# Kernel optimization log

Hardware: AMD Instinct MI355X
Metric: run time of the kernel (lower is better)

Reference implementation:

```python
import jax, jax.numpy as jnp
import numpy as np

EPS = 1e-6
ENERGY_THRESHOLD = 0.95
LS_INIT = 1e-5


def setup_inputs() -> dict:
    key = jax.random.key(0)
    k_x, k_u, k_s, k_v = jax.random.split(key, 4)
    dim, max_rank = 4096, 16
    x = jax.random.normal(k_x, (4, 2048, dim), dtype=jnp.float32)
    U = jax.random.normal(k_u, (dim, max_rank), dtype=jnp.float32) * 0.02
    S = jax.random.uniform(k_s, (max_rank,), dtype=jnp.float32)
    V = jax.random.normal(k_v, (max_rank, dim), dtype=jnp.float32) * 0.02
    norm_weight = jnp.ones((dim,), dtype=jnp.float32)
    gamma = jnp.full((dim,), LS_INIT, dtype=jnp.float32)
    return {"x": x, "U": U, "S": S, "V": V,
            "norm_weight": norm_weight, "gamma": gamma}


def _rank_mask(S):
    # Effective rank from singular-value energy (non-differentiable decision,
    # matching torch's .item() host sync which detaches it from autograd).
    s_abs = jnp.abs(S)
    cum = jnp.cumsum(s_abs) / jnp.maximum(s_abs.sum(), 1e-8)
    hit = cum >= ENERGY_THRESHOLD
    r = jnp.where(hit.any(), jnp.argmax(hit) + 1, S.shape[0])
    keep = (jnp.arange(S.shape[0]) < r).astype(S.dtype)
    return jax.lax.stop_gradient(keep)


def reference(x, U, S, V, norm_weight, gamma):
    # RMSNorm (computed in fp32, matching x.float() in torch)
    xf = x.astype(jnp.float32)
    x_norm = (xf * jax.lax.rsqrt(jnp.mean(xf * xf, axis=-1, keepdims=True) + EPS)).astype(x.dtype)
    x_norm = x_norm * norm_weight
    # Adaptive-rank low-rank projection: masking columns >= r equals slicing [:r]
    keep = _rank_mask(S)
    h = jnp.einsum('bsd,dr->bsr', x_norm, U)        # [B,S,max_rank]
    h = h * (S * keep)                               # zero out ranks >= r
    h = jnp.einsum('bsr,rd->bsd', h, V)             # [B,S,dim]
    # LayerScale + residual
    return x + h * gamma
```

## Files before the change

kernel.cpp:

```cpp
#include <hip/hip_runtime.h>

#define DIM   4096
#define RANK  16
#define BM    16
#define NT    1024
#define NWAVE 16
#define KSLICE (DIM/NWAVE)
#define NKB   (KSLICE/32)
#define NCB   (DIM/16/NWAVE)

typedef __fp16 f16;
typedef __fp16 half4 __attribute__((ext_vector_type(4)));
typedef __fp16 half8 __attribute__((ext_vector_type(8)));
typedef float  floatx4 __attribute__((ext_vector_type(4)));

__global__ __launch_bounds__(256) void prep_weights(const float* __restrict__ U,
    const float* __restrict__ nw, const float* __restrict__ V,
    f16* __restrict__ Ub, f16* __restrict__ Vb)
{
    const int i   = blockIdx.x * 256 + threadIdx.x;
    const int l   = i & 63;
    const int n   = l & 15;
    const int blk = l >> 4;
    if (i < 8192) {
        const int kb = i >> 6;
        half8 u;
        #pragma unroll
        for (int e = 0; e < 8; ++e) {
            const int k = kb * 32 + blk * 8 + e;
            u[e] = (f16)(nw[k] * U[(size_t)k * RANK + n]);
        }
        *(half8*)(Ub + (size_t)i * 8) = u;
    }
    {
        const int cb = i >> 6;
        half4 v;
        #pragma unroll
        for (int e = 0; e < 4; ++e) {
            const int k = blk * 4 + e;
            v[e] = (f16)V[(size_t)k * DIM + cb * 16 + n];
        }
        *(half4*)(Vb + (size_t)i * 4) = v;
    }
}

__global__ __launch_bounds__(NT, 8) void arl_fused(
    const float* __restrict__ x,  const f16* __restrict__ Ub,
    const f16* __restrict__ Vb,   const float* __restrict__ S,
    const float* __restrict__ gamma, float* __restrict__ out)
{
    const int t   = threadIdx.x;
    const int w   = t >> 6;
    const int l   = t & 63;
    const int n   = l & 15;
    const int blk = l >> 4;
    const size_t row0 = (size_t)blockIdx.x * BM;

    __shared__ float s_hacc[NWAVE][16][17];
    __shared__ float s_ssq[NWAVE][16];
    __shared__ __align__(8) f16 s_hh[16][16];

    const float* xlane = x + (row0 + n) * DIM + w * KSLICE + blk * 8;
    const half8* UbW   = (const half8*)Ub + (size_t)w * NKB * 64 + l;

    floatx4 acc = {0.f, 0.f, 0.f, 0.f};
    float ssq = 0.f;

    #pragma unroll
    for (int kb = 0; kb < NKB; ++kb) {
        const float4 xa0 = *(const float4*)(xlane + kb * 32);
        const float4 xa1 = *(const float4*)(xlane + kb * 32 + 4);
        const half8  ub  = UbW[(size_t)kb * 64];
        ssq = fmaf(xa0.x, xa0.x, ssq); ssq = fmaf(xa0.y, xa0.y, ssq);
        ssq = fmaf(xa0.z, xa0.z, ssq); ssq = fmaf(xa0.w, xa0.w, ssq);
        ssq = fmaf(xa1.x, xa1.x, ssq); ssq = fmaf(xa1.y, xa1.y, ssq);
        ssq = fmaf(xa1.z, xa1.z, ssq); ssq = fmaf(xa1.w, xa1.w, ssq);
        half8 a;
        a[0] = (f16)xa0.x; a[1] = (f16)xa0.y; a[2] = (f16)xa0.z; a[3] = (f16)xa0.w;
        a[4] = (f16)xa1.x; a[5] = (f16)xa1.y; a[6] = (f16)xa1.z; a[7] = (f16)xa1.w;
        acc = __builtin_amdgcn_mfma_f32_16x16x32_f16(a, ub, acc, 0, 0, 0);
    }

    ssq += __shfl_xor(ssq, 16, 64);
    ssq += __shfl_xor(ssq, 32, 64);
    if (l < 16) s_ssq[w][l] = ssq;

    #pragma unroll
    for (int j = 0; j < 4; ++j) s_hacc[w][blk * 4 + j][n] = acc[j];
    __syncthreads();

    if (t < 256) {
        const int m = t >> 4, q = t & 15;
        float hsum = 0.f, tssq = 0.f;
        #pragma unroll
        for (int ww = 0; ww < NWAVE; ++ww) {
            hsum += s_hacc[ww][m][q];
            tssq += s_ssq[ww][m];
        }
        const float rstd = rsqrtf(tssq * (1.0f / DIM) + 1e-6f);
        float tot = 0.f;
        #pragma unroll
        for (int i = 0; i < RANK; ++i) tot += fabsf(S[i]);
        const float denom = fmaxf(tot, 1e-8f);
        float cum = 0.f, se = 0.f;
        #pragma unroll
        for (int i = 0; i < RANK; ++i) {
            if (i == q) se = ((cum / denom) < 0.95f) ? S[i] : 0.f;
            cum += fabsf(S[i]);
        }
        s_hh[m][q] = (f16)(hsum * se * rstd);
    }
    __syncthreads();

    const half4 ah = *(const half4*)&s_hh[n][blk * 4];
    const half4* Vb4 = (const half4*)Vb;
    const floatx4 zero = {0.f, 0.f, 0.f, 0.f};

    #pragma unroll 2
    for (int i = 0; i < NCB; ++i) {
        const int cb = w * NCB + i;
        const int c0 = cb * 16;
        const half4 bv = Vb4[(size_t)cb * 64 + l];
        floatx4 d = __builtin_amdgcn_mfma_f32_16x16x16f16(ah, bv, zero, 0, 0, 0);
        const float g = gamma[c0 + n];
        const float* xr  = x   + (row0 + blk * 4) * DIM + c0 + n;
        float*       orr = out + (row0 + blk * 4) * DIM + c0 + n;
        #pragma unroll
        for (int j = 0; j < 4; ++j) {
            const float xv = xr[(size_t)j * DIM];
            __builtin_nontemporal_store(fmaf(g, d[j], xv), orr + (size_t)j * DIM);
        }
    }
}

extern "C" void kernel_launch(void* const* d_in, const int* in_sizes, int n_in,
                              void* d_out, int out_size, void* d_ws, size_t ws_size,
                              hipStream_t stream) {
    (void)in_sizes; (void)n_in; (void)ws_size;
    const float* x  = (const float*)d_in[0];
    const float* U  = (const float*)d_in[1];
    const float* S  = (const float*)d_in[2];
    const float* V  = (const float*)d_in[3];
    const float* nw = (const float*)d_in[4];
    const float* g  = (const float*)d_in[5];
    float* out = (float*)d_out;
    f16* Ub = (f16*)d_ws;
    f16* Vb = (f16*)((char*)d_ws + 128 * 1024);

    hipLaunchKernelGGL(prep_weights, dim3(64), dim3(256), 0, stream,
                       U, nw, V, Ub, Vb);

    const int rows = out_size / DIM;
    const int grid = rows / BM;
    hipLaunchKernelGGL(arl_fused, dim3(grid), dim3(NT), 0, stream,
                       x, Ub, Vb, S, g, out);
}
```

Baseline: 77.37 us.

## Process two row tiles per block, overlapping second projection with first output phase

Each block now handles two 16-row tiles. The reduction loads and MFMA for the second tile are interleaved with the V-projection and residual write of the first tile, so memory traffic and compute from both phases overlap. The output phase also switches to swapped MFMA operands, which lets each lane use float4 loads and stores of x, gamma and out. The grid is halved and the occupancy hint drops from 8 to 4. This risks lower occupancy and more register pressure, and it adds a third barrier.

```diff
diff --git a/kernel.cpp b/kernel.cpp
--- a/kernel.cpp
+++ b/kernel.cpp
@@ -3,16 +3,16 @@
 #define DIM   4096
 #define RANK  16
 #define BM    16
+#define TPB   2
 #define NT    1024
 #define NWAVE 16
-#define KSLICE (DIM/NWAVE)
-#define NKB   (KSLICE/32)
-#define NCB   (DIM/16/NWAVE)
 
 typedef __fp16 f16;
 typedef __fp16 half4 __attribute__((ext_vector_type(4)));
 typedef __fp16 half8 __attribute__((ext_vector_type(8)));
 typedef float  floatx4 __attribute__((ext_vector_type(4)));
+
+#define SCHED_FENCE() __builtin_amdgcn_sched_barrier(0)
 
 __global__ __launch_bounds__(256) void prep_weights(const float* __restrict__ U,
     const float* __restrict__ nw, const float* __restrict__ V,
@@ -44,7 +44,7 @@
     }
 }
 
-__global__ __launch_bounds__(NT, 8) void arl_fused(
+__global__ __launch_bounds__(NT, 4) void arl_fused(
     const float* __restrict__ x,  const f16* __restrict__ Ub,
     const f16* __restrict__ Vb,   const float* __restrict__ S,
     const float* __restrict__ gamma, float* __restrict__ out)
@@ -54,23 +54,27 @@
     const int l   = t & 63;
     const int n   = l & 15;
     const int blk = l >> 4;
-    const size_t row0 = (size_t)blockIdx.x * BM;
+    const size_t rowB = (size_t)blockIdx.x * (BM * TPB);
 
     __shared__ float s_hacc[NWAVE][16][17];
     __shared__ float s_ssq[NWAVE][16];
-    __shared__ __align__(8) f16 s_hh[16][16];
-
-    const float* xlane = x + (row0 + n) * DIM + w * KSLICE + blk * 8;
-    const half8* UbW   = (const half8*)Ub + (size_t)w * NKB * 64 + l;
+    __shared__ __align__(8) f16 s_hh[TPB][16][16];
+
+    const half4* Vb4 = (const half4*)Vb;
+    const floatx4 zero = {0.f, 0.f, 0.f, 0.f};
+
+    const float* xlaneT0 = x + (rowB + n) * DIM + w * 256 + blk * 8;
+    const float* xlaneT1 = xlaneT0 + (size_t)BM * DIM;
+    const f16*   UbW     = Ub + ((size_t)(w * 8) * 64 + l) * 8;
 
     floatx4 acc = {0.f, 0.f, 0.f, 0.f};
     float ssq = 0.f;
 
     #pragma unroll
-    for (int kb = 0; kb < NKB; ++kb) {
-        const float4 xa0 = *(const float4*)(xlane + kb * 32);
-        const float4 xa1 = *(const float4*)(xlane + kb * 32 + 4);
-        const half8  ub  = UbW[(size_t)kb * 64];
+    for (int i = 0; i < 8; ++i) {
+        const float4 xa0 = *(const float4*)(xlaneT0 + i * 32);
+        const float4 xa1 = *(const float4*)(xlaneT0 + i * 32 + 4);
+        const half8  ub  = *(const half8*)(UbW + (size_t)i * 512);
         ssq = fmaf(xa0.x, xa0.x, ssq); ssq = fmaf(xa0.y, xa0.y, ssq);
         ssq = fmaf(xa0.z, xa0.z, ssq); ssq = fmaf(xa0.w, xa0.w, ssq);
         ssq = fmaf(xa1.x, xa1.x, ssq); ssq = fmaf(xa1.y, xa1.y, ssq);
@@ -80,13 +84,14 @@
         a[4] = (f16)xa1.x; a[5] = (f16)xa1.y; a[6] = (f16)xa1.z; a[7] = (f16)xa1.w;
         acc = __builtin_amdgcn_mfma_f32_16x16x32_f16(a, ub, acc, 0, 0, 0);
     }
-
-    ssq += __shfl_xor(ssq, 16, 64);
-    ssq += __shfl_xor(ssq, 32, 64);
-    if (l < 16) s_ssq[w][l] = ssq;
-
-    #pragma unroll
-    for (int j = 0; j < 4; ++j) s_hacc[w][blk * 4 + j][n] = acc[j];
+    {
+        float sq = ssq;
+        sq += __shfl_xor(sq, 16, 64);
+        sq += __shfl_xor(sq, 32, 64);
+        if (l < 16) s_ssq[w][l] = sq;
+        #pragma unroll
+        for (int j = 0; j < 4; ++j) s_hacc[w][blk * 4 + j][n] = acc[j];
+    }
     __syncthreads();
 
     if (t < 256) {
@@ -108,27 +113,102 @@
             if (i == q) se = ((cum / denom) < 0.95f) ? S[i] : 0.f;
             cum += fabsf(S[i]);
         }
-        s_hh[m][q] = (f16)(hsum * se * rstd);
-    }
-    __syncthreads();
-
-    const half4 ah = *(const half4*)&s_hh[n][blk * 4];
-    const half4* Vb4 = (const half4*)Vb;
-    const floatx4 zero = {0.f, 0.f, 0.f, 0.f};
-
-    #pragma unroll 2
-    for (int i = 0; i < NCB; ++i) {
-        const int cb = w * NCB + i;
-        const int c0 = cb * 16;
-        const half4 bv = Vb4[(size_t)cb * 64 + l];
-        floatx4 d = __builtin_amdgcn_mfma_f32_16x16x16f16(ah, bv, zero, 0, 0, 0);
-        const float g = gamma[c0 + n];
-        const float* xr  = x   + (row0 + blk * 4) * DIM + c0 + n;
-        float*       orr = out + (row0 + blk * 4) * DIM + c0 + n;
-        #pragma unroll
-        for (int j = 0; j < 4; ++j) {
-            const float xv = xr[(size_t)j * DIM];
-            __builtin_nontemporal_store(fmaf(g, d[j], xv), orr + (size_t)j * DIM);
+        s_hh[0][m][q] = (f16)(hsum * se * rstd);
+    }
+    __syncthreads();
+
+    acc[0] = 0.f; acc[1] = 0.f; acc[2] = 0.f; acc[3] = 0.f;
+    ssq = 0.f;
+    {
+        const half4 ah0  = *(const half4*)&s_hh[0][n][blk * 4];
+        const float* xrow0 = x   + (rowB + n) * DIM;
+        float*       orow0 = out + (rowB + n) * DIM;
+
+        #pragma unroll 1
+        for (int i = 0; i < 8; ++i) {
+            const float4 xa0 = *(const float4*)(xlaneT1 + i * 32);
+            const float4 xa1 = *(const float4*)(xlaneT1 + i * 32 + 4);
+            const half8  ub  = *(const half8*)(UbW + (size_t)i * 512);
+            SCHED_FENCE();
+
+            #pragma unroll
+            for (int c = 0; c < 2; ++c) {
+                const int cb = w * 16 + 2 * i + c;
+                const int c0 = cb * 16 + blk * 4;
+                const half4 bv = Vb4[(size_t)cb * 64 + l];
+                floatx4 d = __builtin_amdgcn_mfma_f32_16x16x16f16(bv, ah0, zero, 0, 0, 0);
+                const float4 g  = *(const float4*)(gamma + c0);
+                const float4 xv = *(const float4*)(xrow0 + c0);
+                floatx4 o;
+                o[0] = fmaf(g.x, d[0], xv.x);
+                o[1] = fmaf(g.y, d[1], xv.y);
+                o[2] = fmaf(g.z, d[2], xv.z);
+                o[3] = fmaf(g.w, d[3], xv.w);
+                __builtin_nontemporal_store(o, (floatx4*)(orow0 + c0));
+            }
+
+            ssq = fmaf(xa0.x, xa0.x, ssq); ssq = fmaf(xa0.y, xa0.y, ssq);
+            ssq = fmaf(xa0.z, xa0.z, ssq); ssq = fmaf(xa0.w, xa0.w, ssq);
+            ssq = fmaf(xa1.x, xa1.x, ssq); ssq = fmaf(xa1.y, xa1.y, ssq);
+            ssq = fmaf(xa1.z, xa1.z, ssq); ssq = fmaf(xa1.w, xa1.w, ssq);
+            half8 a;
+            a[0] = (f16)xa0.x; a[1] = (f16)xa0.y; a[2] = (f16)xa0.z; a[3] = (f16)xa0.w;
+            a[4] = (f16)xa1.x; a[5] = (f16)xa1.y; a[6] = (f16)xa1.z; a[7] = (f16)xa1.w;
+            acc = __builtin_amdgcn_mfma_f32_16x16x32_f16(a, ub, acc, 0, 0, 0);
+        }
+    }
+    {
+        float sq = ssq;
+        sq += __shfl_xor(sq, 16, 64);
+        sq += __shfl_xor(sq, 32, 64);
+        if (l < 16) s_ssq[w][l] = sq;
+    }
+    __syncthreads();
+    #pragma unroll
+    for (int j = 0; j < 4; ++j) s_hacc[w][blk * 4 + j][n] = acc[j];
+    __syncthreads();
+
+    if (t < 256) {
+        const int m = t >> 4, q = t & 15;
+        float hsum = 0.f, tssq = 0.f;
+        #pragma unroll
+        for (int ww = 0; ww < NWAVE; ++ww) {
+            hsum += s_hacc[ww][m][q];
+            tssq += s_ssq[ww][m];
+        }
+        const float rstd = rsqrtf(tssq * (1.0f / DIM) + 1e-6f);
+        float tot = 0.f;
+        #pragma unroll
+        for (int i = 0; i < RANK; ++i) tot += fabsf(S[i]);
+        const float denom = fmaxf(tot, 1e-8f);
+        float cum = 0.f, se = 0.f;
+        #pragma unroll
+        for (int i = 0; i < RANK; ++i) {
+            if (i == q) se = ((cum / denom) < 0.95f) ? S[i] : 0.f;
+            cum += fabsf(S[i]);
+        }
+        s_hh[1][m][q] = (f16)(hsum * se * rstd);
+    }
+    __syncthreads();
+
+    {
+        const half4 ah1  = *(const half4*)&s_hh[1][n][blk * 4];
+        const float* xrow1 = x   + (rowB + BM + n) * DIM;
+        float*       orow1 = out + (rowB + BM + n) * DIM;
+        #pragma unroll 4
+        for (int i = 0; i < 16; ++i) {
+            const int cb = w * 16 + i;
+            const int c0 = cb * 16 + blk * 4;
+            const half4 bv = Vb4[(size_t)cb * 64 + l];
+            floatx4 d = __builtin_amdgcn_mfma_f32_16x16x16f16(bv, ah1, zero, 0, 0, 0);
+            const float4 g  = *(const float4*)(gamma + c0);
+            const float4 xv = *(const float4*)(xrow1 + c0);
+            floatx4 o;
+            o[0] = fmaf(g.x, d[0], xv.x);
+            o[1] = fmaf(g.y, d[1], xv.y);
+            o[2] = fmaf(g.z, d[2], xv.z);
+            o[3] = fmaf(g.w, d[3], xv.w);
+            __builtin_nontemporal_store(o, (floatx4*)(orow1 + c0));
         }
     }
 }
@@ -151,7 +231,7 @@
                        U, nw, V, Ub, Vb);
 
     const int rows = out_size / DIM;
-    const int grid = rows / BM;
+    const int grid = rows / (BM * TPB);
     hipLaunchKernelGGL(arl_fused, dim3(grid), dim3(NT), 0, stream,
                        x, Ub, Vb, S, g, out);
 }
```

Result: slower. 82.25 us (+6.3%).
